# Optimization experiments

Measured on AMD Instinct MI355X. Metric: run time of the kernel, lower is better.

Reference implementation:

```python
import jax, jax.numpy as jnp
import numpy as np

EMBED_SIZE = 1024
HEADS = 16
HEAD_DIM = EMBED_SIZE // HEADS


def setup_inputs() -> dict:
    key = jax.random.key(0)
    k1, k2, k3, k4 = jax.random.split(key, 4)
    N, L = 4, 2048
    return {
        "values": jax.random.normal(k1, (N, L, EMBED_SIZE), dtype=jnp.float32),
        "keys": jax.random.normal(k2, (N, L, EMBED_SIZE), dtype=jnp.float32),
        "query": jax.random.normal(k3, (N, L, EMBED_SIZE), dtype=jnp.float32),
        "w_out": jax.random.normal(k4, (EMBED_SIZE, EMBED_SIZE), dtype=jnp.float32) * (1.0 / np.sqrt(EMBED_SIZE)),
        "b_out": jnp.zeros((EMBED_SIZE,), dtype=jnp.float32),
    }


def reference(values, keys, query, w_out, b_out):
    N, q_len, _ = query.shape
    v_len = values.shape[1]
    k_len = keys.shape[1]
    # split heads: (N, L, H, D). NOTE: source never applies the per-head
    # q/k/v Linear layers in forward, so raw inputs are used directly.
    v = values.reshape(N, v_len, HEADS, HEAD_DIM)
    k = keys.reshape(N, k_len, HEADS, HEAD_DIM)
    q = query.reshape(N, q_len, HEADS, HEAD_DIM)
    # energy: (N, H, Q, K); scale by sqrt(embed_size) as in the source
    energy = jnp.einsum('nqhd,nkhd->nhqk', q, k)
    attn = jax.nn.softmax(energy / jnp.sqrt(jnp.float32(EMBED_SIZE)), axis=3)
    out = jnp.einsum('nhql,nlhd->nqhd', attn, v).reshape(N, q_len, EMBED_SIZE)
    # fc_out: x @ W.T + b (torch Linear convention)
    return out @ w_out.T + b_out
```

## Files before the change

kernel.cpp:

```cpp
#include <hip/hip_runtime.h>
#include <hip/hip_bf16.h>

#define NB 4
#define LSEQ 2048
#define NH 16
#define HD 64
#define EMB 1024

typedef __attribute__((ext_vector_type(8))) short bf16x8;
typedef __attribute__((ext_vector_type(4))) float f32x4;
typedef __attribute__((ext_vector_type(16))) float f32x16;
typedef __attribute__((ext_vector_type(2))) unsigned int uint2v;

__device__ __forceinline__ unsigned short f2bf(float x) {
    union { float f; unsigned u; } v; v.f = x;
    unsigned r = v.u + 0x7fff + ((v.u >> 16) & 1);
    return (unsigned short)(r >> 16);
}

__device__ __forceinline__ float exp2_fast(float x) {
#if __has_builtin(__builtin_amdgcn_exp2f)
    return __builtin_amdgcn_exp2f(x);
#else
    float r; asm("v_exp_f32 %0, %1\n\ts_nop 1" : "=v"(r) : "v"(x)); return r;
#endif
}

__device__ __forceinline__ unsigned pack_bf2(float lo, float hi) {
    union { __hip_bfloat162 h2; unsigned u; } cv;
    cv.h2 = __float22bfloat162_rn(make_float2(lo, hi));
    return cv.u;
}

__device__ __forceinline__ void plswap(unsigned &a, unsigned &b) {
#if __has_builtin(__builtin_amdgcn_permlane32_swap)
    uint2v r = __builtin_amdgcn_permlane32_swap(a, b, false, false);
    a = r[0]; b = r[1];
#else
    asm volatile("s_nop 0\n\tv_permlane32_swap_b32 %0, %1\n\ts_nop 0"
                 : "+v"(a), "+v"(b));
#endif
}

__device__ __forceinline__ void async16(void* lds, const void* g) {
    __builtin_amdgcn_global_load_lds(
        (const __attribute__((address_space(1))) unsigned int*)g,
        (__attribute__((address_space(3))) unsigned int*)lds, 16, 0, 0);
}

__global__ void wconv_kernel(const float* __restrict__ Wf, unsigned short* __restrict__ Wb) {
    int i = (blockIdx.x * 256 + threadIdx.x) * 4;
    float4 v = *(const float4*)(Wf + i);
    ushort4 o = { f2bf(v.x), f2bf(v.y), f2bf(v.z), f2bf(v.w) };
    *(ushort4*)(Wb + i) = o;
}

__global__ void k_prep(const float* __restrict__ Kf, unsigned short* __restrict__ Kb) {
    int idx = blockIdx.x * 256 + threadIdx.x;
    int c   = idx & 7;
    int key = (idx >> 3) & 2047;
    int h   = (idx >> 14) & 15;
    int n   = idx >> 18;
    const float* src = Kf + (size_t)(n * LSEQ + key) * EMB + h * HD + c * 8;
    float4 a = *(const float4*)src;
    float4 b = *(const float4*)(src + 4);
    unsigned short* dst = Kb + (((size_t)(n * NH + h) * LSEQ + key) << 6)
                             + ((c ^ (key & 7)) << 3);
    ushort4 o0 = { f2bf(a.x), f2bf(a.y), f2bf(a.z), f2bf(a.w) };
    ushort4 o1 = { f2bf(b.x), f2bf(b.y), f2bf(b.z), f2bf(b.w) };
    *(ushort4*)dst = o0;
    *(ushort4*)(dst + 4) = o1;
}

__global__ void v_prep2(const float* __restrict__ Vf, unsigned short* __restrict__ Vt) {
    __shared__ float T[64][65];
    const int tid = threadIdx.x;
    const int b = blockIdx.x;
    const int kt = b & 31, h = (b >> 5) & 15, n = b >> 9;
    const float* src = Vf + (size_t)(n * LSEQ + kt * 64) * EMB + h * HD;
    unsigned short* dst = Vt + ((size_t)b << 12);

    for (int i = tid; i < 1024; i += 256) {
        const int key = i >> 4;
        const int c4  = (i & 15) * 4;
        const float4 v = *(const float4*)(src + (size_t)key * EMB + c4);
        T[key][c4 + 0] = v.x; T[key][c4 + 1] = v.y;
        T[key][c4 + 2] = v.z; T[key][c4 + 3] = v.w;
    }
    __syncthreads();
    for (int i = tid; i < 512; i += 256) {
        const int d = i >> 3, c = i & 7;
        ushort4 o0 = { f2bf(T[c * 8 + 0][d]), f2bf(T[c * 8 + 1][d]),
                       f2bf(T[c * 8 + 2][d]), f2bf(T[c * 8 + 3][d]) };
        ushort4 o1 = { f2bf(T[c * 8 + 4][d]), f2bf(T[c * 8 + 5][d]),
                       f2bf(T[c * 8 + 6][d]), f2bf(T[c * 8 + 7][d]) };
        unsigned short* p = dst + (d << 6) + ((c ^ (d & 7)) << 3);
        *(ushort4*)p = o0;
        *(ushort4*)(p + 4) = o1;
    }
}

__global__ __launch_bounds__(256, 2)
void attn9_kernel(const float* __restrict__ Qq, const unsigned short* __restrict__ Kb,
                  const unsigned short* __restrict__ Vt, unsigned short* __restrict__ X)
{
    __shared__ unsigned short Kl[2][8192];
    __shared__ unsigned short Vl[2][8192];

    const int tid  = threadIdx.x;
    const int lane = tid & 63;
    const int w    = tid >> 6;
    const int l31  = lane & 31;
    const int hl   = lane >> 5;
    const int swz7 = lane & 7;
    const int l    = ((blockIdx.x & 7) << 6) + (blockIdx.x >> 3);
    const int nh   = l >> 3;
    const int qtile = l & 7;
    const int n = nh >> 4, h = nh & 15;
    const int qrow0 = qtile * 256 + w * 64;

    const float qscale = 0.03125f * 1.44269504f;
    bf16x8 qf[2][4];
    #pragma unroll
    for (int g = 0; g < 2; ++g) {
        const float* qp = Qq + (size_t)(n * LSEQ + qrow0 + g * 32 + l31) * EMB + h * HD + hl * 8;
        #pragma unroll
        for (int dk = 0; dk < 4; ++dk) {
            bf16x8 t;
            #pragma unroll
            for (int e = 0; e < 8; ++e) t[e] = (short)f2bf(qp[dk * 16 + e] * qscale);
            qf[g][dk] = t;
        }
    }

    f32x16 oaccT[2][2];
    #pragma unroll
    for (int g = 0; g < 2; ++g)
        #pragma unroll
        for (int db = 0; db < 2; ++db)
            #pragma unroll
            for (int e = 0; e < 16; ++e) oaccT[g][db][e] = 0.f;
    float lp[2] = {0.f, 0.f};

    const unsigned short* kg0 = Kb + ((size_t)nh << 17);
    const unsigned short* vg0 = Vt + ((size_t)nh << 17);
    const int t8 = tid << 3;

#define ATTN_STAGE(buf, kt)                                                  \
    {                                                                        \
        const unsigned short* kg = kg0 + ((kt) << 13) + t8;                  \
        const unsigned short* vg = vg0 + ((kt) << 13) + t8;                  \
        _Pragma("unroll")                                                    \
        for (int j = 0; j < 4; ++j) {                                        \
            async16(&Kl[buf][t8 + j * 2048], kg + j * 2048);                 \
            async16(&Vl[buf][t8 + j * 2048], vg + j * 2048);                 \
        }                                                                    \
    }

    ATTN_STAGE(0, 0)
    asm volatile("s_waitcnt vmcnt(0)" ::: "memory");
    __syncthreads();

    int cur = 0;
    for (int kt = 0; kt < LSEQ / 128; ++kt) {
        if (kt + 1 < LSEQ / 128) ATTN_STAGE(cur ^ 1, kt + 1)

        #pragma unroll
        for (int kb = 0; kb < 4; ++kb) {
            f32x16 sk[2];
            #pragma unroll
            for (int g = 0; g < 2; ++g)
                #pragma unroll
                for (int e = 0; e < 16; ++e) sk[g][e] = 0.f;
            __builtin_amdgcn_s_setprio(1);
            #pragma unroll
            for (int dk = 0; dk < 4; ++dk) {
                bf16x8 ka = *(const bf16x8*)&Kl[cur][((kb * 32 + l31) << 6) + (((2 * dk + hl) ^ swz7) << 3)];
                #pragma unroll
                for (int g = 0; g < 2; ++g)
                    sk[g] = __builtin_amdgcn_mfma_f32_32x32x16_bf16(ka, qf[g][dk], sk[g], 0, 0, 0);
            }
            __builtin_amdgcn_s_setprio(0);

            unsigned wgt[2][4][2];
            #pragma unroll
            for (int g = 0; g < 2; ++g) {
                float p[16];
                #pragma unroll
                for (int e = 0; e < 16; ++e) p[e] = exp2_fast(sk[g][e]);
                {
                    float t0 = (p[0] + p[1]) + (p[2] + p[3]);
                    float t1 = (p[4] + p[5]) + (p[6] + p[7]);
                    float t2 = (p[8] + p[9]) + (p[10] + p[11]);
                    float t3 = (p[12] + p[13]) + (p[14] + p[15]);
                    lp[g] += (t0 + t1) + (t2 + t3);
                }
                #pragma unroll
                for (int gg = 0; gg < 4; ++gg) {
                    wgt[g][gg][0] = pack_bf2(p[4 * gg + 0], p[4 * gg + 1]);
                    wgt[g][gg][1] = pack_bf2(p[4 * gg + 2], p[4 * gg + 3]);
                }
                plswap(wgt[g][0][0], wgt[g][1][0]); plswap(wgt[g][0][1], wgt[g][1][1]);
                plswap(wgt[g][2][0], wgt[g][3][0]); plswap(wgt[g][2][1], wgt[g][3][1]);
            }

            const int vbase = (kb >> 1) << 12;
            const int kb1   = kb & 1;
            __builtin_amdgcn_s_setprio(1);
            #pragma unroll
            for (int ks = 0; ks < 2; ++ks) {
                #pragma unroll
                for (int db = 0; db < 2; ++db) {
                    bf16x8 va = *(const bf16x8*)&Vl[cur][vbase + ((db * 32 + l31) << 6) + (((4 * kb1 + 2 * ks + hl) ^ swz7) << 3)];
                    #pragma unroll
                    for (int g = 0; g < 2; ++g) {
                        union { unsigned u[4]; bf16x8 v; } pu;
                        pu.u[0] = wgt[g][2 * ks + 0][0];
                        pu.u[1] = wgt[g][2 * ks + 0][1];
                        pu.u[2] = wgt[g][2 * ks + 1][0];
                        pu.u[3] = wgt[g][2 * ks + 1][1];
                        oaccT[g][db] = __builtin_amdgcn_mfma_f32_32x32x16_bf16(va, pu.v, oaccT[g][db], 0, 0, 0);
                    }
                }
            }
            __builtin_amdgcn_s_setprio(0);
        }

        asm volatile("s_waitcnt vmcnt(0)" ::: "memory");
        __syncthreads();
        cur ^= 1;
    }

    #pragma unroll
    for (int g = 0; g < 2; ++g) {
        const float ltot = lp[g] + __shfl_xor(lp[g], 32);
        const float rcp = 1.0f / ltot;
        unsigned ow0[4][2], ow1[4][2];
        #pragma unroll
        for (int gg = 0; gg < 4; ++gg) {
            ow0[gg][0] = pack_bf2(oaccT[g][0][4 * gg + 0] * rcp, oaccT[g][0][4 * gg + 1] * rcp);
            ow0[gg][1] = pack_bf2(oaccT[g][0][4 * gg + 2] * rcp, oaccT[g][0][4 * gg + 3] * rcp);
            ow1[gg][0] = pack_bf2(oaccT[g][1][4 * gg + 0] * rcp, oaccT[g][1][4 * gg + 1] * rcp);
            ow1[gg][1] = pack_bf2(oaccT[g][1][4 * gg + 2] * rcp, oaccT[g][1][4 * gg + 3] * rcp);
        }
        #pragma unroll
        for (int gg = 0; gg < 4; ++gg) {
            plswap(ow0[gg][0], ow1[gg][0]);
            plswap(ow0[gg][1], ow1[gg][1]);
        }
        unsigned short* xrow = X + (size_t)(n * LSEQ + qrow0 + g * 32 + l31) * EMB + h * HD + hl * 32;
        #pragma unroll
        for (int gg = 0; gg < 4; ++gg) {
            uint4 st = { ow0[gg][0], ow0[gg][1], ow1[gg][0], ow1[gg][1] };
            *(uint4*)(xrow + 8 * gg) = st;
        }
    }
}

#define KPAD 72
#define PPAD 72

__global__ __launch_bounds__(256, 2)
void attn_kernel(const float* __restrict__ Vv, const float* __restrict__ Kk,
                 const float* __restrict__ Qq, unsigned short* __restrict__ X)
{
    __shared__ unsigned short Klds[64 * KPAD];
    __shared__ unsigned short Vtlds[64 * KPAD];
    __shared__ unsigned short Plds[4 * 16 * PPAD];

    const int tid  = threadIdx.x;
    const int lane = tid & 63;
    const int w    = tid >> 6;
    const int l15  = lane & 15;
    const int l4   = lane >> 4;
    const int qtile = blockIdx.x;
    const int nh    = blockIdx.y;
    const int n = nh >> 4, h = nh & 15;

    bf16x8 qf[2];
    {
        const int qrow = qtile * 64 + w * 16 + l15;
        const float* qp = Qq + (size_t)(n * LSEQ + qrow) * EMB + h * HD + l4 * 8;
        for (int kk = 0; kk < 2; ++kk) {
            bf16x8 t;
            #pragma unroll
            for (int e = 0; e < 8; ++e) t[e] = (short)f2bf(qp[kk * 32 + e] * 0.03125f);
            qf[kk] = t;
        }
    }

    f32x4 oacc[4];
    #pragma unroll
    for (int f = 0; f < 4; ++f) oacc[f] = (f32x4){0.f, 0.f, 0.f, 0.f};
    float mrun[4], lrun[4];
    #pragma unroll
    for (int r = 0; r < 4; ++r) { mrun[r] = -1e30f; lrun[r] = 0.f; }

    for (int kt = 0; kt < LSEQ / 64; ++kt) {
        __syncthreads();
        for (int i = tid; i < 1024; i += 256) {
            const int row = i >> 4;
            const int c4  = (i & 15) * 4;
            const size_t gb = (size_t)(n * LSEQ + kt * 64 + row) * EMB + h * HD + c4;
            const float4 kv = *(const float4*)(Kk + gb);
            const float4 vv = *(const float4*)(Vv + gb);
            ushort4 k4 = { f2bf(kv.x), f2bf(kv.y), f2bf(kv.z), f2bf(kv.w) };
            *(ushort4*)&Klds[row * KPAD + c4] = k4;
            Vtlds[(c4 + 0) * KPAD + row] = f2bf(vv.x);
            Vtlds[(c4 + 1) * KPAD + row] = f2bf(vv.y);
            Vtlds[(c4 + 2) * KPAD + row] = f2bf(vv.z);
            Vtlds[(c4 + 3) * KPAD + row] = f2bf(vv.w);
        }
        __syncthreads();

        f32x4 s[4];
        #pragma unroll
        for (int f = 0; f < 4; ++f) {
            f32x4 acc = (f32x4){0.f, 0.f, 0.f, 0.f};
            #pragma unroll
            for (int kk = 0; kk < 2; ++kk) {
                bf16x8 kb = *(const bf16x8*)&Klds[(f * 16 + l15) * KPAD + kk * 32 + l4 * 8];
                acc = __builtin_amdgcn_mfma_f32_16x16x32_bf16(qf[kk], kb, acc, 0, 0, 0);
            }
            s[f] = acc;
        }

        float mnew[4], corr[4];
        #pragma unroll
        for (int r = 0; r < 4; ++r) {
            float m0 = fmaxf(fmaxf(s[0][r], s[1][r]), fmaxf(s[2][r], s[3][r]));
            #pragma unroll
            for (int msk = 1; msk < 16; msk <<= 1) m0 = fmaxf(m0, __shfl_xor(m0, msk));
            mnew[r] = fmaxf(mrun[r], m0);
            corr[r] = __expf(mrun[r] - mnew[r]);
        }
        float psum[4] = {0.f, 0.f, 0.f, 0.f};
        #pragma unroll
        for (int f = 0; f < 4; ++f) {
            #pragma unroll
            for (int r = 0; r < 4; ++r) {
                float p = __expf(s[f][r] - mnew[r]);
                psum[r] += p;
                Plds[(w * 16 + l4 * 4 + r) * PPAD + f * 16 + l15] = f2bf(p);
            }
        }
        #pragma unroll
        for (int r = 0; r < 4; ++r) {
            float t = psum[r];
            #pragma unroll
            for (int msk = 1; msk < 16; msk <<= 1) t += __shfl_xor(t, msk);
            lrun[r] = lrun[r] * corr[r] + t;
            mrun[r] = mnew[r];
        }
        #pragma unroll
        for (int f = 0; f < 4; ++f) {
            #pragma unroll
            for (int r = 0; r < 4; ++r) oacc[f][r] *= corr[r];
        }
        __syncthreads();

        #pragma unroll
        for (int ks = 0; ks < 2; ++ks) {
            bf16x8 pa = *(const bf16x8*)&Plds[(w * 16 + l15) * PPAD + ks * 32 + l4 * 8];
            #pragma unroll
            for (int f = 0; f < 4; ++f) {
                bf16x8 vb = *(const bf16x8*)&Vtlds[(f * 16 + l15) * KPAD + ks * 32 + l4 * 8];
                oacc[f] = __builtin_amdgcn_mfma_f32_16x16x32_bf16(pa, vb, oacc[f], 0, 0, 0);
            }
        }
    }

    #pragma unroll
    for (int f = 0; f < 4; ++f) {
        #pragma unroll
        for (int r = 0; r < 4; ++r) {
            const int qrow = qtile * 64 + w * 16 + l4 * 4 + r;
            const float o = oacc[f][r] / lrun[r];
            X[(size_t)(n * LSEQ + qrow) * EMB + h * HD + f * 16 + l15] = f2bf(o);
        }
    }
}

__global__ __launch_bounds__(256, 2)
void proj4_kernel(const unsigned short* __restrict__ X, const unsigned short* __restrict__ Wb,
                  const float* __restrict__ bias, float* __restrict__ out)
{
    __shared__ unsigned short Al[2][8192];
    __shared__ unsigned short Bl[2][8192];

    const int tid  = threadIdx.x;
    const int lane = tid & 63;
    const int w    = tid >> 6;
    const int l15  = lane & 15;
    const int l4   = lane >> 4;
    const int bid  = blockIdx.x;
    const int bm   = (bid & 7) * 8 + ((bid >> 3) & 7);
    const int bn   = bid >> 6;
    const int wr = (w >> 1) * 64;
    const int wc = (w & 1) * 64;

    f32x4 acc[4][4];
    #pragma unroll
    for (int i = 0; i < 4; ++i)
        #pragma unroll
        for (int j = 0; j < 4; ++j) acc[i][j] = (f32x4){0.f, 0.f, 0.f, 0.f};

    int srow[4], soff[4];
    #pragma unroll
    for (int j = 0; j < 4; ++j) {
        const int cid = tid + j * 256;
        srow[j] = cid >> 3;
        const int c = cid & 7;
        soff[j] = ((c ^ (srow[j] & 7)) << 3);
    }

#define PROJ_STAGE(buf, k0)                                                          \
    {                                                                                \
        _Pragma("unroll")                                                            \
        for (int j = 0; j < 4; ++j) {                                                \
            const int cid = tid + j * 256;                                           \
            async16(&Al[buf][cid << 3],                                              \
                    &X [(size_t)(bm * 128 + srow[j]) * EMB + (k0) + soff[j]]);       \
            async16(&Bl[buf][cid << 3],                                              \
                    &Wb[(size_t)(bn * 128 + srow[j]) * EMB + (k0) + soff[j]]);       \
        }                                                                            \
    }

    PROJ_STAGE(0, 0)
    asm volatile("s_waitcnt vmcnt(0)" ::: "memory");
    __syncthreads();

    int cur = 0;
    for (int k0 = 0; k0 < EMB; k0 += 64) {
        if (k0 + 64 < EMB) PROJ_STAGE(cur ^ 1, k0 + 64)

        #pragma unroll
        for (int kk = 0; kk < 2; ++kk) {
            bf16x8 af[4], bfr[4];
            #pragma unroll
            for (int i = 0; i < 4; ++i) {
                const int row = wr + i * 16 + l15;
                af[i] = *(const bf16x8*)&Al[cur][(row << 6) + (((kk * 4 + l4) ^ (row & 7)) << 3)];
            }
            #pragma unroll
            for (int j = 0; j < 4; ++j) {
                const int row = wc + j * 16 + l15;
                bfr[j] = *(const bf16x8*)&Bl[cur][(row << 6) + (((kk * 4 + l4) ^ (row & 7)) << 3)];
            }
            __builtin_amdgcn_s_setprio(1);
            #pragma unroll
            for (int i = 0; i < 4; ++i)
                #pragma unroll
                for (int j = 0; j < 4; ++j)
                    acc[i][j] = __builtin_amdgcn_mfma_f32_16x16x32_bf16(af[i], bfr[j], acc[i][j], 0, 0, 0);
            __builtin_amdgcn_s_setprio(0);
        }

        asm volatile("s_waitcnt vmcnt(0)" ::: "memory");
        __syncthreads();
        cur ^= 1;
    }

    #pragma unroll
    for (int i = 0; i < 4; ++i) {
        const int row = bm * 128 + wr + i * 16 + l4 * 4;
        #pragma unroll
        for (int j = 0; j < 4; ++j) {
            const int col = bn * 128 + wc + j * 16 + l15;
            const float bj = bias[col];
            #pragma unroll
            for (int r = 0; r < 4; ++r)
                out[(size_t)(row + r) * EMB + col] = acc[i][j][r] + bj;
        }
    }
}

extern "C" void kernel_launch(void* const* d_in, const int* in_sizes, int n_in,
                              void* d_out, int out_size, void* d_ws, size_t ws_size,
                              hipStream_t stream) {
    const float* Vv   = (const float*)d_in[0];
    const float* Kk   = (const float*)d_in[1];
    const float* Qq   = (const float*)d_in[2];
    const float* Wf   = (const float*)d_in[3];
    const float* bias = (const float*)d_in[4];
    float* out = (float*)d_out;

    unsigned short* X  = (unsigned short*)d_ws;
    unsigned short* Wb = (unsigned short*)((char*)d_ws + (size_t)16 * 1024 * 1024);
    const size_t need = (size_t)50 * 1024 * 1024;

    wconv_kernel<<<dim3(EMB * EMB / 1024), 256, 0, stream>>>(Wf, Wb);

    if (ws_size >= need) {
        unsigned short* Kb = (unsigned short*)((char*)d_ws + (size_t)18 * 1024 * 1024);
        unsigned short* Vt = (unsigned short*)((char*)d_ws + (size_t)34 * 1024 * 1024);
        k_prep<<<dim3(4096), 256, 0, stream>>>(Kk, Kb);
        v_prep2<<<dim3(2048), 256, 0, stream>>>(Vv, Vt);
        attn9_kernel<<<dim3(512), 256, 0, stream>>>(Qq, Kb, Vt, X);
    } else {
        attn_kernel<<<dim3(LSEQ / 64, NB * NH), 256, 0, stream>>>(Vv, Kk, Qq, X);
    }

    proj4_kernel<<<dim3(512), 256, 0, stream>>>(X, Wb, bias, out);
}
```

Before: 137.9 us.

## Compute softmax row sums via MFMA with ones vector and halve key tile

The attention kernel now accumulates the softmax denominator with an extra MFMA that multiplies the bf16 probabilities by a vector of ones, replacing the per-lane VALU reduction and the cross-lane shuffle. The key/value tile per stage drops from 128 to 64 keys, halving LDS use and doubling the number of loop iterations and barriers. The s_setprio hints are also removed from both the attention and projection kernels. The denominator is now summed from bf16-rounded weights, which matches the numerator's rounding but adds MFMA work, and the smaller tiles raise synchronisation overhead in exchange for possibly higher occupancy.

```diff
diff --git a/kernel.cpp b/kernel.cpp
--- a/kernel.cpp
+++ b/kernel.cpp
@@ -101,11 +101,11 @@
 }
 
 __global__ __launch_bounds__(256, 2)
-void attn9_kernel(const float* __restrict__ Qq, const unsigned short* __restrict__ Kb,
-                  const unsigned short* __restrict__ Vt, unsigned short* __restrict__ X)
+void attn11_kernel(const float* __restrict__ Qq, const unsigned short* __restrict__ Kb,
+                   const unsigned short* __restrict__ Vt, unsigned short* __restrict__ X)
 {
-    __shared__ unsigned short Kl[2][8192];
-    __shared__ unsigned short Vl[2][8192];
+    __shared__ unsigned short Kl[2][4096];
+    __shared__ unsigned short Vl[2][4096];
 
     const int tid  = threadIdx.x;
     const int lane = tid & 63;
@@ -119,6 +119,10 @@
     const int n = nh >> 4, h = nh & 15;
     const int qrow0 = qtile * 256 + w * 64;
 
+    bf16x8 ones;
+    #pragma unroll
+    for (int e = 0; e < 8; ++e) ones[e] = (short)0x3F80;
+
     const float qscale = 0.03125f * 1.44269504f;
     bf16x8 qf[2][4];
     #pragma unroll
@@ -134,45 +138,46 @@
     }
 
     f32x16 oaccT[2][2];
-    #pragma unroll
-    for (int g = 0; g < 2; ++g)
+    f32x16 lacc[2];
+    #pragma unroll
+    for (int g = 0; g < 2; ++g) {
+        #pragma unroll
+        for (int e = 0; e < 16; ++e) lacc[g][e] = 0.f;
         #pragma unroll
         for (int db = 0; db < 2; ++db)
             #pragma unroll
             for (int e = 0; e < 16; ++e) oaccT[g][db][e] = 0.f;
-    float lp[2] = {0.f, 0.f};
+    }
 
     const unsigned short* kg0 = Kb + ((size_t)nh << 17);
     const unsigned short* vg0 = Vt + ((size_t)nh << 17);
     const int t8 = tid << 3;
 
-#define ATTN_STAGE(buf, kt)                                                  \
-    {                                                                        \
-        const unsigned short* kg = kg0 + ((kt) << 13) + t8;                  \
-        const unsigned short* vg = vg0 + ((kt) << 13) + t8;                  \
-        _Pragma("unroll")                                                    \
-        for (int j = 0; j < 4; ++j) {                                        \
-            async16(&Kl[buf][t8 + j * 2048], kg + j * 2048);                 \
-            async16(&Vl[buf][t8 + j * 2048], vg + j * 2048);                 \
-        }                                                                    \
-    }
-
-    ATTN_STAGE(0, 0)
+    async16(&Kl[0][t8],        kg0 + t8);
+    async16(&Kl[0][t8 + 2048], kg0 + t8 + 2048);
+    async16(&Vl[0][t8],        vg0 + t8);
+    async16(&Vl[0][t8 + 2048], vg0 + t8 + 2048);
     asm volatile("s_waitcnt vmcnt(0)" ::: "memory");
     __syncthreads();
 
     int cur = 0;
-    for (int kt = 0; kt < LSEQ / 128; ++kt) {
-        if (kt + 1 < LSEQ / 128) ATTN_STAGE(cur ^ 1, kt + 1)
-
-        #pragma unroll
-        for (int kb = 0; kb < 4; ++kb) {
+    for (int kt = 0; kt < LSEQ / 64; ++kt) {
+        if (kt + 1 < LSEQ / 64) {
+            const unsigned short* kg = kg0 + ((kt + 1) << 12) + t8;
+            const unsigned short* vg = vg0 + ((kt + 1) << 12) + t8;
+            async16(&Kl[cur ^ 1][t8],        kg);
+            async16(&Kl[cur ^ 1][t8 + 2048], kg + 2048);
+            async16(&Vl[cur ^ 1][t8],        vg);
+            async16(&Vl[cur ^ 1][t8 + 2048], vg + 2048);
+        }
+
+        #pragma unroll
+        for (int kb = 0; kb < 2; ++kb) {
             f32x16 sk[2];
             #pragma unroll
             for (int g = 0; g < 2; ++g)
                 #pragma unroll
                 for (int e = 0; e < 16; ++e) sk[g][e] = 0.f;
-            __builtin_amdgcn_s_setprio(1);
             #pragma unroll
             for (int dk = 0; dk < 4; ++dk) {
                 bf16x8 ka = *(const bf16x8*)&Kl[cur][((kb * 32 + l31) << 6) + (((2 * dk + hl) ^ swz7) << 3)];
@@ -180,7 +185,6 @@
                 for (int g = 0; g < 2; ++g)
                     sk[g] = __builtin_amdgcn_mfma_f32_32x32x16_bf16(ka, qf[g][dk], sk[g], 0, 0, 0);
             }
-            __builtin_amdgcn_s_setprio(0);
 
             unsigned wgt[2][4][2];
             #pragma unroll
@@ -188,13 +192,6 @@
                 float p[16];
                 #pragma unroll
                 for (int e = 0; e < 16; ++e) p[e] = exp2_fast(sk[g][e]);
-                {
-                    float t0 = (p[0] + p[1]) + (p[2] + p[3]);
-                    float t1 = (p[4] + p[5]) + (p[6] + p[7]);
-                    float t2 = (p[8] + p[9]) + (p[10] + p[11]);
-                    float t3 = (p[12] + p[13]) + (p[14] + p[15]);
-                    lp[g] += (t0 + t1) + (t2 + t3);
-                }
                 #pragma unroll
                 for (int gg = 0; gg < 4; ++gg) {
                     wgt[g][gg][0] = pack_bf2(p[4 * gg + 0], p[4 * gg + 1]);
@@ -204,26 +201,25 @@
                 plswap(wgt[g][2][0], wgt[g][3][0]); plswap(wgt[g][2][1], wgt[g][3][1]);
             }
 
-            const int vbase = (kb >> 1) << 12;
-            const int kb1   = kb & 1;
-            __builtin_amdgcn_s_setprio(1);
             #pragma unroll
             for (int ks = 0; ks < 2; ++ks) {
+                union { unsigned u[4]; bf16x8 v; } pu[2];
+                #pragma unroll
+                for (int g = 0; g < 2; ++g) {
+                    pu[g].u[0] = wgt[g][2 * ks + 0][0];
+                    pu[g].u[1] = wgt[g][2 * ks + 0][1];
+                    pu[g].u[2] = wgt[g][2 * ks + 1][0];
+                    pu[g].u[3] = wgt[g][2 * ks + 1][1];
+                    lacc[g] = __builtin_amdgcn_mfma_f32_32x32x16_bf16(ones, pu[g].v, lacc[g], 0, 0, 0);
+                }
                 #pragma unroll
                 for (int db = 0; db < 2; ++db) {
-                    bf16x8 va = *(const bf16x8*)&Vl[cur][vbase + ((db * 32 + l31) << 6) + (((4 * kb1 + 2 * ks + hl) ^ swz7) << 3)];
+                    bf16x8 va = *(const bf16x8*)&Vl[cur][((db * 32 + l31) << 6) + (((4 * kb + 2 * ks + hl) ^ swz7) << 3)];
                     #pragma unroll
-                    for (int g = 0; g < 2; ++g) {
-                        union { unsigned u[4]; bf16x8 v; } pu;
-                        pu.u[0] = wgt[g][2 * ks + 0][0];
-                        pu.u[1] = wgt[g][2 * ks + 0][1];
-                        pu.u[2] = wgt[g][2 * ks + 1][0];
-                        pu.u[3] = wgt[g][2 * ks + 1][1];
-                        oaccT[g][db] = __builtin_amdgcn_mfma_f32_32x32x16_bf16(va, pu.v, oaccT[g][db], 0, 0, 0);
-                    }
+                    for (int g = 0; g < 2; ++g)
+                        oaccT[g][db] = __builtin_amdgcn_mfma_f32_32x32x16_bf16(va, pu[g].v, oaccT[g][db], 0, 0, 0);
                 }
             }
-            __builtin_amdgcn_s_setprio(0);
         }
 
         asm volatile("s_waitcnt vmcnt(0)" ::: "memory");
@@ -233,8 +229,7 @@
 
     #pragma unroll
     for (int g = 0; g < 2; ++g) {
-        const float ltot = lp[g] + __shfl_xor(lp[g], 32);
-        const float rcp = 1.0f / ltot;
+        const float rcp = 1.0f / lacc[g][0];
         unsigned ow0[4][2], ow1[4][2];
         #pragma unroll
         for (int gg = 0; gg < 4; ++gg) {
@@ -447,13 +442,11 @@
                 const int row = wc + j * 16 + l15;
                 bfr[j] = *(const bf16x8*)&Bl[cur][(row << 6) + (((kk * 4 + l4) ^ (row & 7)) << 3)];
             }
-            __builtin_amdgcn_s_setprio(1);
             #pragma unroll
             for (int i = 0; i < 4; ++i)
                 #pragma unroll
                 for (int j = 0; j < 4; ++j)
                     acc[i][j] = __builtin_amdgcn_mfma_f32_16x16x32_bf16(af[i], bfr[j], acc[i][j], 0, 0, 0);
-            __builtin_amdgcn_s_setprio(0);
         }
 
         asm volatile("s_waitcnt vmcnt(0)" ::: "memory");
@@ -496,7 +489,7 @@
         unsigned short* Vt = (unsigned short*)((char*)d_ws + (size_t)34 * 1024 * 1024);
         k_prep<<<dim3(4096), 256, 0, stream>>>(Kk, Kb);
         v_prep2<<<dim3(2048), 256, 0, stream>>>(Vv, Vt);
-        attn9_kernel<<<dim3(512), 256, 0, stream>>>(Qq, Kb, Vt, X);
+        attn11_kernel<<<dim3(512), 256, 0, stream>>>(Qq, Kb, Vt, X);
     } else {
         attn_kernel<<<dim3(LSEQ / 64, NB * NH), 256, 0, stream>>>(Vv, Kk, Qq, X);
     }
```

Measured after the change: 131.5 us. 4.6% less time.
